# Kernel optimization log

Hardware: AMD Instinct MI355X
Metric: run time of the kernel (lower is better)

Reference implementation:

```python
import jax, jax.numpy as jnp
import numpy as np

B, S, E = 4, 2048, 1024


def setup_inputs() -> dict:
    key = jax.random.key(0)
    k1, k2, k3, k4 = jax.random.split(key, 4)
    scale = 1.0 / np.sqrt(E)
    return {
        "x": jax.random.normal(k1, (B, S, E), dtype=jnp.float32),
        "W_Q": jax.random.normal(k2, (E, E), dtype=jnp.float32) * scale,
        "W_K": jax.random.normal(k3, (E, E), dtype=jnp.float32) * scale,
        "W_V": jax.random.normal(k4, (E, E), dtype=jnp.float32) * scale,
    }


def reference(x, W_Q, W_K, W_V):
    # nn.Linear(E, E, bias=False): y = x @ W.T
    Q = jnp.einsum("bse,fe->bsf", x, W_Q)
    K = jnp.einsum("bse,fe->bsf", x, W_K)
    V = jnp.einsum("bse,fe->bsf", x, W_V)
    d = Q.shape[-1]
    scores = jnp.einsum("bqd,bkd->bqk", Q, K) / jnp.sqrt(jnp.float32(d))
    # causal mask: -inf strictly above the diagonal
    seq = Q.shape[1]
    causal = jnp.tril(jnp.ones((seq, seq), dtype=bool))  # [S,S]
    scores = jnp.where(causal[None, :, :], scores, jnp.float32(-jnp.inf))
    attn = jax.nn.softmax(scores, axis=-1)
    return jnp.einsum("bqk,bkd->bqd", attn, V)
```

## Files before the change

kernel.cpp:

```cpp
#include <hip/hip_runtime.h>
#include <hip/hip_bf16.h>
#include <stdint.h>

typedef __hip_bfloat16 bf16;
typedef __attribute__((ext_vector_type(8))) short bf16x8;
typedef __attribute__((ext_vector_type(4))) float f32x4;
typedef __attribute__((ext_vector_type(8))) unsigned short u16x8;
typedef __attribute__((ext_vector_type(4))) unsigned short u16x4;

#define SLEN 2048
#define ED   1024
#define NB   4
#define AS1 __attribute__((address_space(1)))
#define AS3 __attribute__((address_space(3)))
#define SB0() __builtin_amdgcn_sched_barrier(0)

static __device__ __forceinline__ unsigned short f2bf(float f) {
    return __builtin_bit_cast(unsigned short, __float2bfloat16(f));
}

__device__ __forceinline__ void gemm_core(
    const char* __restrict__ aT, int lda,
    const char* __restrict__ bT, int ldb,
    int nkt, char* sm, int tid, f32x4 (&acc)[4][4])
{
    const int lane = tid & 63, wave = tid >> 6;
    const int wm = wave >> 1, wn = wave & 1;
    const int fr = lane & 15, kc = lane >> 4;

    auto STAGE = [&](int kh, int Tn) {
        char* buf = sm + (Tn & 1) * 49152;
#pragma unroll
        for (int j = 0; j < 2; ++j) {
            int rid = j * 512 + tid;
            int row = rid >> 2, c = rid & 3;
            const char* src = aT + (size_t)row * lda + Tn * 128 + kh * 64
                            + ((c ^ ((row >> 1) & 3)) * 16);
            __builtin_amdgcn_global_load_lds(
                (const AS1 uint32_t*)src,
                (AS3 uint32_t*)(buf + kh * 16384 + (j * 512 + wave * 64) * 16),
                16, 0, 0);
        }
        {
            int row = tid >> 2, c = tid & 3;
            const char* src = bT + (size_t)row * ldb + Tn * 128 + kh * 64
                            + ((c ^ ((row >> 1) & 3)) * 16);
            __builtin_amdgcn_global_load_lds(
                (const AS1 uint32_t*)src,
                (AS3 uint32_t*)(buf + 32768 + kh * 8192 + (wave * 64) * 16),
                16, 0, 0);
        }
    };
    auto RD = [&](int T, int kh, bf16x8 (&a)[4], bf16x8 (&b)[4]) {
        const char* buf = sm + (T & 1) * 49152;
#pragma unroll
        for (int i = 0; i < 4; ++i) {
            int row = wm * 64 + i * 16 + fr;
            a[i] = *(const bf16x8*)(buf + kh * 16384 + row * 64
                                    + ((kc ^ ((row >> 1) & 3)) * 16));
        }
#pragma unroll
        for (int i = 0; i < 4; ++i) {
            int row = wn * 64 + i * 16 + fr;
            b[i] = *(const bf16x8*)(buf + 32768 + kh * 8192 + row * 64
                                    + ((kc ^ ((row >> 1) & 3)) * 16));
        }
    };
    auto MM = [&](bf16x8 (&a)[4], bf16x8 (&b)[4]) {
        __builtin_amdgcn_s_setprio(1);
#pragma unroll
        for (int i = 0; i < 4; ++i)
#pragma unroll
            for (int n = 0; n < 4; ++n)
                acc[i][n] = __builtin_amdgcn_mfma_f32_16x16x32_bf16(
                    a[i], b[n], acc[i][n], 0, 0, 0);
        __builtin_amdgcn_s_setprio(0);
    };

    STAGE(0, 0); STAGE(1, 0);
    asm volatile("s_waitcnt vmcnt(3)" ::: "memory");
    SB0();
    __builtin_amdgcn_s_barrier();

    bf16x8 aE[4], bE[4], aO[4], bO[4];
    for (int T = 0; T < nkt; ++T) {
        const bool pre = (T + 1 < nkt);
        RD(T, 0, aE, bE);
        SB0();
        if (pre) STAGE(0, T + 1);
        SB0();
        if (T > 0) {
            asm volatile("s_waitcnt lgkmcnt(8)" ::: "memory");
            SB0();
            MM(aO, bO);
        }
        if (pre) asm volatile("s_waitcnt vmcnt(3)" ::: "memory");
        else     asm volatile("s_waitcnt vmcnt(0)" ::: "memory");
        SB0();
        __builtin_amdgcn_s_barrier();
        RD(T, 1, aO, bO);
        SB0();
        if (pre) STAGE(1, T + 1);
        SB0();
        asm volatile("s_waitcnt lgkmcnt(8)" ::: "memory");
        SB0();
        MM(aE, bE);
        if (pre) asm volatile("s_waitcnt vmcnt(3)" ::: "memory");
        else     asm volatile("s_waitcnt vmcnt(0)" ::: "memory");
        SB0();
        __builtin_amdgcn_s_barrier();
    }
    asm volatile("s_waitcnt lgkmcnt(0)" ::: "memory");
    SB0();
    MM(aO, bO);
}

__global__ __launch_bounds__(256) void convert_to_bf16(
    const float* __restrict__ x, const float* __restrict__ wq,
    const float* __restrict__ wk, const float* __restrict__ wv,
    bf16* __restrict__ xb, bf16* __restrict__ wqb,
    bf16* __restrict__ wkb, bf16* __restrict__ wvb)
{
    long g = (long)blockIdx.x * 256 + threadIdx.x;
    const float* src; bf16* dst; long o;
    if (g < 1048576) { src = x; dst = xb; o = g * 8; }
    else {
        long g2 = g - 1048576;
        int w = (int)(g2 >> 17);
        o = (g2 & 131071) * 8;
        src = (w == 0) ? wq : (w == 1) ? wk : wv;
        dst = (w == 0) ? wqb : (w == 1) ? wkb : wvb;
    }
    float4 v0 = *(const float4*)(src + o);
    float4 v1 = *(const float4*)(src + o + 4);
    u16x8 r;
    r[0] = f2bf(v0.x); r[1] = f2bf(v0.y); r[2] = f2bf(v0.z); r[3] = f2bf(v0.w);
    r[4] = f2bf(v1.x); r[5] = f2bf(v1.y); r[6] = f2bf(v1.z); r[7] = f2bf(v1.w);
    *(u16x8*)(dst + o) = r;
}

__global__ __launch_bounds__(512, 2) void qkv_gemm(
    const bf16* __restrict__ xb, const bf16* __restrict__ wqb,
    const bf16* __restrict__ wkb, const bf16* __restrict__ wvb,
    bf16* __restrict__ Qb, bf16* __restrict__ Kb, bf16* __restrict__ Vt)
{
    extern __shared__ char smem[];
    int bid = blockIdx.x, tid = threadIdx.x;
    int xcd = bid & 7, i = bid >> 3;
    int tm = (xcd << 2) | (i & 3);
    int tn = i >> 2;
    const bf16* W = (tn < 8) ? wqb : (tn < 16) ? wkb : wvb;
    int tnl = tn & 7;
    f32x4 acc[4][4] = {};
    gemm_core((const char*)(xb + (size_t)tm * 256 * ED), ED * 2,
              (const char*)(W + (size_t)tnl * 128 * ED), ED * 2,
              16, smem, tid, acc);

    int lane = tid & 63, wave = tid >> 6, wm = wave >> 1, wn = wave & 1;
    int rl = (lane >> 4) * 4, cl = lane & 15;
    if (tn < 16) {
        bf16* C = (tn < 8) ? Qb : Kb;
#pragma unroll
        for (int mf = 0; mf < 4; ++mf)
#pragma unroll
            for (int j = 0; j < 4; ++j) {
                int r = tm * 256 + wm * 64 + mf * 16 + rl + j;
#pragma unroll
                for (int nf = 0; nf < 4; ++nf) {
                    int c = tnl * 128 + wn * 64 + nf * 16 + cl;
                    C[(size_t)r * ED + c] = __float2bfloat16(acc[mf][nf][j]);
                }
            }
    } else {
#pragma unroll
        for (int mf = 0; mf < 4; ++mf)
#pragma unroll
            for (int j = 0; j < 4; ++j) {
                int r = tm * 256 + wm * 64 + mf * 16 + rl + j;
                int bb = r >> 11, s = r & 2047;
#pragma unroll
                for (int nf = 0; nf < 4; ++nf) {
                    int d = tnl * 128 + wn * 64 + nf * 16 + cl;
                    Vt[(((size_t)bb << 10) + d) * SLEN + s] = __float2bfloat16(acc[mf][nf][j]);
                }
            }
    }
}

__global__ __launch_bounds__(512, 2) void qk_gemm(
    const bf16* __restrict__ Qb, const bf16* __restrict__ Kb, float* __restrict__ Sc)
{
    extern __shared__ char smem[];
    int bx = blockIdx.x, b = blockIdx.y, tid = threadIdx.x;
    int t = (bx & 7) * 9 + (bx >> 3);
    int ti = 0;
    while ((ti + 1) * (ti + 2) <= t) ++ti;
    int tj = t - ti * (ti + 1);
    f32x4 acc[4][4] = {};
    gemm_core((const char*)(Qb + ((size_t)b * SLEN + ti * 256) * ED), ED * 2,
              (const char*)(Kb + ((size_t)b * SLEN + tj * 128) * ED), ED * 2,
              16, smem, tid, acc);

    float* Sb = Sc + (size_t)b * SLEN * SLEN;
    int lane = tid & 63, wave = tid >> 6, wm = wave >> 1, wn = wave & 1;
    int rl = (lane >> 4) * 4, cl = lane & 15;
#pragma unroll
    for (int mf = 0; mf < 4; ++mf)
#pragma unroll
        for (int j = 0; j < 4; ++j) {
            int r = ti * 256 + wm * 64 + mf * 16 + rl + j;
#pragma unroll
            for (int nf = 0; nf < 4; ++nf) {
                int c = tj * 128 + wn * 64 + nf * 16 + cl;
                Sb[(size_t)r * SLEN + c] = acc[mf][nf][j] * 0.03125f;
            }
        }
}

__global__ __launch_bounds__(256) void softmax_rows(float* __restrict__ Sc)
{
    int q = blockIdx.x, b = blockIdx.y, tid = threadIdx.x;
    float* row = Sc + ((size_t)b * SLEN + q) * SLEN;
    int lane = tid & 63, wave = tid >> 6;
    __shared__ float red[4];

    float vals[8];
    float lmax = -3.0e38f;
#pragma unroll
    for (int r = 0; r < 2; ++r) {
        int i4 = tid + r * 256;
        if (i4 * 4 <= q) {
            float4 v = *(const float4*)(row + i4 * 4);
            vals[r * 4 + 0] = v.x; vals[r * 4 + 1] = v.y;
            vals[r * 4 + 2] = v.z; vals[r * 4 + 3] = v.w;
#pragma unroll
            for (int e = 0; e < 4; ++e) {
                int k = i4 * 4 + e;
                if (k <= q) lmax = fmaxf(lmax, vals[r * 4 + e]);
            }
        }
    }
#pragma unroll
    for (int o = 32; o > 0; o >>= 1) lmax = fmaxf(lmax, __shfl_xor(lmax, o));
    if (lane == 0) red[wave] = lmax;
    __syncthreads();
    float m = fmaxf(fmaxf(red[0], red[1]), fmaxf(red[2], red[3]));
    __syncthreads();
    float lsum = 0.f;
#pragma unroll
    for (int r = 0; r < 2; ++r) {
        int i4 = tid + r * 256;
        if (i4 * 4 <= q)
#pragma unroll
            for (int e = 0; e < 4; ++e) {
                int k = i4 * 4 + e;
                if (k <= q) lsum += __expf(vals[r * 4 + e] - m);
            }
    }
#pragma unroll
    for (int o = 32; o > 0; o >>= 1) lsum += __shfl_xor(lsum, o);
    if (lane == 0) red[wave] = lsum;
    __syncthreads();
    float inv = 1.0f / (red[0] + red[1] + red[2] + red[3]);
    unsigned short* prow = (unsigned short*)row;
#pragma unroll
    for (int r = 0; r < 2; ++r) {
        int i4 = tid + r * 256;
        u16x4 o4;
#pragma unroll
        for (int e = 0; e < 4; ++e) {
            int k = i4 * 4 + e;
            float p = (k <= q) ? __expf(vals[r * 4 + e] - m) * inv : 0.0f;
            o4[e] = f2bf(p);
        }
        *(u16x4*)(prow + i4 * 4) = o4;
    }
}

__global__ __launch_bounds__(512, 2) void pv_gemm(
    const bf16* __restrict__ P, const bf16* __restrict__ Vt, float* __restrict__ O)
{
    extern __shared__ char smem[];
    int mq = 7 - blockIdx.x, nd = blockIdx.y, b = blockIdx.z, tid = threadIdx.x;
    f32x4 acc[4][4] = {};
    int nkt = (mq + 1) * 4;
    gemm_core((const char*)P + ((size_t)b * SLEN + mq * 256) * 8192, 8192,
              (const char*)(Vt + ((size_t)b * ED + nd * 128) * SLEN), SLEN * 2,
              nkt, smem, tid, acc);

    int lane = tid & 63, wave = tid >> 6, wm = wave >> 1, wn = wave & 1;
    int rl = (lane >> 4) * 4, cl = lane & 15;
    float* Ob = O + (size_t)b * SLEN * ED;
#pragma unroll
    for (int mf = 0; mf < 4; ++mf)
#pragma unroll
        for (int j = 0; j < 4; ++j) {
            int r = mq * 256 + wm * 64 + mf * 16 + rl + j;
#pragma unroll
            for (int nf = 0; nf < 4; ++nf) {
                int c = nd * 128 + wn * 64 + nf * 16 + cl;
                Ob[(size_t)r * ED + c] = acc[mf][nf][j];
            }
        }
}

extern "C" void kernel_launch(void* const* d_in, const int* in_sizes, int n_in,
                              void* d_out, int out_size, void* d_ws, size_t ws_size,
                              hipStream_t stream)
{
    const float* x  = (const float*)d_in[0];
    const float* wq = (const float*)d_in[1];
    const float* wk = (const float*)d_in[2];
    const float* wv = (const float*)d_in[3];
    float* out = (float*)d_out;

    char* ws = (char*)d_ws;
    bf16* xb  = (bf16*)(ws);
    bf16* wqb = (bf16*)(ws + 16777216);
    bf16* wkb = (bf16*)(ws + 18874368);
    bf16* wvb = (bf16*)(ws + 20971520);
    bf16* Qb  = (bf16*)(ws + 23068672);
    bf16* Kb  = (bf16*)(ws + 39845888);
    bf16* Vt  = (bf16*)(ws + 56623104);
    float* Sc = (float*)(ws + 73400320);

    (void)hipFuncSetAttribute((const void*)qkv_gemm,
            hipFuncAttributeMaxDynamicSharedMemorySize, 98304);
    (void)hipFuncSetAttribute((const void*)qk_gemm,
            hipFuncAttributeMaxDynamicSharedMemorySize, 98304);
    (void)hipFuncSetAttribute((const void*)pv_gemm,
            hipFuncAttributeMaxDynamicSharedMemorySize, 98304);

    convert_to_bf16<<<5632, 256, 0, stream>>>(x, wq, wk, wv, xb, wqb, wkb, wvb);
    qkv_gemm<<<768, 512, 98304, stream>>>(xb, wqb, wkb, wvb, Qb, Kb, Vt);
    qk_gemm<<<dim3(72, NB), 512, 98304, stream>>>(Qb, Kb, Sc);
    softmax_rows<<<dim3(SLEN, NB), 256, 0, stream>>>(Sc);
    pv_gemm<<<dim3(8, 8, NB), 512, 98304, stream>>>((const bf16*)Sc, Vt, out);
}
```

Before: 155.1 us.

## Rebalance causal PV GEMM with smaller tiles and an atomic work queue

Replaces the 256x128, 512-thread PV GEMM with a 128x128, 256-thread variant that has its own two-stage LDS pipeline (gemm2p). Blocks pull tiles from a global atomic counter, heaviest causal rows first, to cut the load imbalance from triangular work. The counter lives in the no-longer-needed W_K bf16 workspace slot and is reset by an extra memset each call. Smaller tiles lower per-tile data reuse and add atomic and barrier overhead.

```diff
diff --git a/kernel.cpp b/kernel.cpp
--- a/kernel.cpp
+++ b/kernel.cpp
@@ -19,7 +19,7 @@
     return __builtin_bit_cast(unsigned short, __float2bfloat16(f));
 }
 
-__device__ __forceinline__ void gemm_core(
+__device__ __forceinline__ void gemm_core8(
     const char* __restrict__ aT, int lda,
     const char* __restrict__ bT, int ldb,
     int nkt, char* sm, int tid, f32x4 (&acc)[4][4])
@@ -115,6 +115,79 @@
     MM(aO, bO);
 }
 
+__device__ __forceinline__ void gemm2p(
+    const char* __restrict__ aT, int lda,
+    const char* __restrict__ bT, int ldb,
+    int nkt, char* sm, int tid, f32x4 (&acc)[4][4])
+{
+    const int lane = tid & 63, wave = tid >> 6;
+    const int wm = wave >> 1, wn = wave & 1;
+    const int fr = lane & 15, kc = lane >> 4;
+
+    auto STAGE = [&](int kh, int Tn) {
+        char* base = sm + (Tn & 1) * 32768 + kh * 8192;
+#pragma unroll
+        for (int half = 0; half < 2; ++half) {
+            const char* g = half ? bT : aT;
+            const int ld = half ? ldb : lda;
+            char* pb = base + half * 16384;
+#pragma unroll
+            for (int j = 0; j < 2; ++j) {
+                int rid = j * 256 + tid;
+                int row = rid >> 2, c = rid & 3;
+                const char* src = g + (size_t)row * ld + Tn * 128 + kh * 64
+                                + ((c ^ ((row >> 1) & 3)) * 16);
+                __builtin_amdgcn_global_load_lds(
+                    (const AS1 uint32_t*)src,
+                    (AS3 uint32_t*)(pb + (j * 256 + wave * 64) * 16),
+                    16, 0, 0);
+            }
+        }
+    };
+
+    STAGE(0, 0); STAGE(1, 0);
+    asm volatile("s_waitcnt vmcnt(4)" ::: "memory");
+    __builtin_amdgcn_sched_barrier(0);
+    __builtin_amdgcn_s_barrier();
+
+    for (int T = 0; T < nkt; ++T) {
+        const bool pre = (T + 1 < nkt);
+#pragma unroll
+        for (int kh = 0; kh < 2; ++kh) {
+            const char* buf = sm + (T & 1) * 32768 + kh * 8192;
+            bf16x8 a[4], b[4];
+#pragma unroll
+            for (int i = 0; i < 4; ++i) {
+                int row = wm * 64 + i * 16 + fr;
+                a[i] = *(const bf16x8*)(buf + row * 64 + ((kc ^ ((row >> 1) & 3)) * 16));
+            }
+#pragma unroll
+            for (int i = 0; i < 4; ++i) {
+                int row = wn * 64 + i * 16 + fr;
+                b[i] = *(const bf16x8*)(buf + 16384 + row * 64 + ((kc ^ ((row >> 1) & 3)) * 16));
+            }
+            if (pre) {
+                STAGE(kh, T + 1);
+                asm volatile("s_waitcnt vmcnt(4)" ::: "memory");
+            } else {
+                asm volatile("s_waitcnt vmcnt(0)" ::: "memory");
+            }
+            __builtin_amdgcn_sched_barrier(0);
+            __builtin_amdgcn_s_barrier();
+            asm volatile("s_waitcnt lgkmcnt(0)" ::: "memory");
+            __builtin_amdgcn_sched_barrier(0);
+            __builtin_amdgcn_s_setprio(1);
+#pragma unroll
+            for (int i = 0; i < 4; ++i)
+#pragma unroll
+                for (int n = 0; n < 4; ++n)
+                    acc[i][n] = __builtin_amdgcn_mfma_f32_16x16x32_bf16(
+                        a[i], b[n], acc[i][n], 0, 0, 0);
+            __builtin_amdgcn_s_setprio(0);
+        }
+    }
+}
+
 __global__ __launch_bounds__(256) void convert_to_bf16(
     const float* __restrict__ x, const float* __restrict__ wq,
     const float* __restrict__ wk, const float* __restrict__ wv,
@@ -152,9 +225,9 @@
     const bf16* W = (tn < 8) ? wqb : (tn < 16) ? wkb : wvb;
     int tnl = tn & 7;
     f32x4 acc[4][4] = {};
-    gemm_core((const char*)(xb + (size_t)tm * 256 * ED), ED * 2,
-              (const char*)(W + (size_t)tnl * 128 * ED), ED * 2,
-              16, smem, tid, acc);
+    gemm_core8((const char*)(xb + (size_t)tm * 256 * ED), ED * 2,
+               (const char*)(W + (size_t)tnl * 128 * ED), ED * 2,
+               16, smem, tid, acc);
 
     int lane = tid & 63, wave = tid >> 6, wm = wave >> 1, wn = wave & 1;
     int rl = (lane >> 4) * 4, cl = lane & 15;
@@ -197,9 +270,9 @@
     while ((ti + 1) * (ti + 2) <= t) ++ti;
     int tj = t - ti * (ti + 1);
     f32x4 acc[4][4] = {};
-    gemm_core((const char*)(Qb + ((size_t)b * SLEN + ti * 256) * ED), ED * 2,
-              (const char*)(Kb + ((size_t)b * SLEN + tj * 128) * ED), ED * 2,
-              16, smem, tid, acc);
+    gemm_core8((const char*)(Qb + ((size_t)b * SLEN + ti * 256) * ED), ED * 2,
+               (const char*)(Kb + ((size_t)b * SLEN + tj * 128) * ED), ED * 2,
+               16, smem, tid, acc);
 
     float* Sb = Sc + (size_t)b * SLEN * SLEN;
     int lane = tid & 63, wave = tid >> 6, wm = wave >> 1, wn = wave & 1;
@@ -277,31 +350,42 @@
     }
 }
 
-__global__ __launch_bounds__(512, 2) void pv_gemm(
-    const bf16* __restrict__ P, const bf16* __restrict__ Vt, float* __restrict__ O)
+__global__ __launch_bounds__(256, 2) void pv_gemm(
+    const bf16* __restrict__ P, const bf16* __restrict__ Vt,
+    float* __restrict__ O, int* __restrict__ ctr)
 {
     extern __shared__ char smem[];
-    int mq = 7 - blockIdx.x, nd = blockIdx.y, b = blockIdx.z, tid = threadIdx.x;
-    f32x4 acc[4][4] = {};
-    int nkt = (mq + 1) * 4;
-    gemm_core((const char*)P + ((size_t)b * SLEN + mq * 256) * 8192, 8192,
-              (const char*)(Vt + ((size_t)b * ED + nd * 128) * SLEN), SLEN * 2,
-              nkt, smem, tid, acc);
-
-    int lane = tid & 63, wave = tid >> 6, wm = wave >> 1, wn = wave & 1;
-    int rl = (lane >> 4) * 4, cl = lane & 15;
-    float* Ob = O + (size_t)b * SLEN * ED;
-#pragma unroll
-    for (int mf = 0; mf < 4; ++mf)
-#pragma unroll
-        for (int j = 0; j < 4; ++j) {
-            int r = mq * 256 + wm * 64 + mf * 16 + rl + j;
-#pragma unroll
-            for (int nf = 0; nf < 4; ++nf) {
-                int c = nd * 128 + wn * 64 + nf * 16 + cl;
-                Ob[(size_t)r * ED + c] = acc[mf][nf][j];
-            }
-        }
+    __shared__ int tsh;
+    int tid = threadIdx.x;
+    for (;;) {
+        __syncthreads();
+        if (tid == 0) tsh = atomicAdd(ctr, 1);
+        __syncthreads();
+        int t = tsh;
+        if (t >= 512) break;
+        int mq = 15 - (t >> 5), sub = t & 31;
+        int nd = sub >> 2, b = sub & 3;
+        f32x4 acc[4][4] = {};
+        int nkt = (mq + 1) * 2;
+        gemm2p((const char*)P + ((size_t)b * SLEN + mq * 128) * 8192, 8192,
+               (const char*)(Vt + ((size_t)b * ED + nd * 128) * SLEN), SLEN * 2,
+               nkt, smem, tid, acc);
+
+        int lane = tid & 63, wave = tid >> 6, wm = wave >> 1, wn = wave & 1;
+        int rl = (lane >> 4) * 4, cl = lane & 15;
+        float* Ob = O + (size_t)b * SLEN * ED;
+#pragma unroll
+        for (int mf = 0; mf < 4; ++mf)
+#pragma unroll
+            for (int j = 0; j < 4; ++j) {
+                int r = mq * 128 + wm * 64 + mf * 16 + rl + j;
+#pragma unroll
+                for (int nf = 0; nf < 4; ++nf) {
+                    int c = nd * 128 + wn * 64 + nf * 16 + cl;
+                    Ob[(size_t)r * ED + c] = acc[mf][nf][j];
+                }
+            }
+    }
 }
 
 extern "C" void kernel_launch(void* const* d_in, const int* in_sizes, int n_in,
@@ -323,17 +407,19 @@
     bf16* Kb  = (bf16*)(ws + 39845888);
     bf16* Vt  = (bf16*)(ws + 56623104);
     float* Sc = (float*)(ws + 73400320);
+    int*  ctr = (int*)(ws + 18874368);
 
     (void)hipFuncSetAttribute((const void*)qkv_gemm,
             hipFuncAttributeMaxDynamicSharedMemorySize, 98304);
     (void)hipFuncSetAttribute((const void*)qk_gemm,
             hipFuncAttributeMaxDynamicSharedMemorySize, 98304);
     (void)hipFuncSetAttribute((const void*)pv_gemm,
-            hipFuncAttributeMaxDynamicSharedMemorySize, 98304);
+            hipFuncAttributeMaxDynamicSharedMemorySize, 65536);
 
     convert_to_bf16<<<5632, 256, 0, stream>>>(x, wq, wk, wv, xb, wqb, wkb, wvb);
     qkv_gemm<<<768, 512, 98304, stream>>>(xb, wqb, wkb, wvb, Qb, Kb, Vt);
     qk_gemm<<<dim3(72, NB), 512, 98304, stream>>>(Qb, Kb, Sc);
     softmax_rows<<<dim3(SLEN, NB), 256, 0, stream>>>(Sc);
-    pv_gemm<<<dim3(8, 8, NB), 512, 98304, stream>>>((const bf16*)Sc, Vt, out);
-}
+    (void)hipMemsetAsync(ctr, 0, sizeof(int), stream);
+    pv_gemm<<<512, 256, 65536, stream>>>((const bf16*)Sc, Vt, out, ctr);
+}
```

New measurement: 235.9 us. 52.1% more time.

## Use 256x256 tiles with 8-phase pipelined GEMM for QKV and QK kernels

Applied to the files above, without the earlier changes.

Adds a new GEMM core that computes 256x256 output tiles per block, with 8 waves each owning 128x64, and interleaves LDS reads, MFMA and async global-to-LDS staging across sub-phases with barriers and priority hints. The QKV projection and QK score kernels switch to this core, halving their grid sizes and using 128KB of shared memory. The aim is higher arithmetic intensity per LDS byte and better overlap of loads with compute. In exchange, occupancy drops to one block per CU, and the QK causal tiling now computes full 256-wide diagonal tiles.

```diff
diff --git a/kernel.cpp b/kernel.cpp
--- a/kernel.cpp
+++ b/kernel.cpp
@@ -19,7 +19,100 @@
     return __builtin_bit_cast(unsigned short, __float2bfloat16(f));
 }
 
-__device__ __forceinline__ void gemm_core(
+__device__ __forceinline__ void gemm8p(
+    const char* __restrict__ aT, int lda,
+    const char* __restrict__ bT, int ldb,
+    int nkt, char* sm, int tid, f32x4 (&acc)[8][4])
+{
+    const int lane = tid & 63, wave = tid >> 6;
+    const int wm = wave >> 2, wn = wave & 3;
+    const int fr = lane & 15, kc = lane >> 4;
+
+    auto SU = [&](int isB, int kh, int Tn) {
+        char* dst = sm + (Tn & 1) * 65536 + isB * 32768 + kh * 16384;
+        const char* g = isB ? bT : aT;
+        const int ld = isB ? ldb : lda;
+#pragma unroll
+        for (int j = 0; j < 2; ++j) {
+            int rid = j * 512 + tid;
+            int row = rid >> 2, c = rid & 3;
+            const char* src = g + (size_t)row * ld + Tn * 128 + kh * 64
+                            + ((c ^ ((row >> 1) & 3)) * 16);
+            __builtin_amdgcn_global_load_lds(
+                (const AS1 uint32_t*)src,
+                (AS3 uint32_t*)(dst + (j * 512 + wave * 64) * 16), 16, 0, 0);
+        }
+    };
+    auto RDA = [&](int T, int kh, bf16x8 (&a)[8]) {
+        const char* pa = sm + (T & 1) * 65536 + kh * 16384;
+#pragma unroll
+        for (int i = 0; i < 8; ++i) {
+            int row = wm * 128 + i * 16 + fr;
+            a[i] = *(const bf16x8*)(pa + row * 64 + ((kc ^ ((row >> 1) & 3)) * 16));
+        }
+    };
+    auto RDB = [&](int T, int kh, int nh, bf16x8 (&b)[2]) {
+        const char* pb = sm + (T & 1) * 65536 + 32768 + kh * 16384;
+#pragma unroll
+        for (int n = 0; n < 2; ++n) {
+            int row = wn * 64 + nh * 32 + n * 16 + fr;
+            b[n] = *(const bf16x8*)(pb + row * 64 + ((kc ^ ((row >> 1) & 3)) * 16));
+        }
+    };
+    auto MM = [&](bf16x8 (&a)[8], bf16x8 (&b)[2], int nh) {
+        __builtin_amdgcn_s_setprio(1);
+#pragma unroll
+        for (int i = 0; i < 8; ++i)
+#pragma unroll
+            for (int n = 0; n < 2; ++n)
+                acc[i][nh * 2 + n] = __builtin_amdgcn_mfma_f32_16x16x32_bf16(
+                    a[i], b[n], acc[i][nh * 2 + n], 0, 0, 0);
+        __builtin_amdgcn_s_setprio(0);
+    };
+
+    SU(0, 0, 0); SU(1, 0, 0); SU(0, 1, 0); SU(1, 1, 0);
+    SU(0, 0, 1); SU(1, 0, 1); SU(0, 1, 1);
+    asm volatile("s_waitcnt vmcnt(6)" ::: "memory");
+    SB0();
+    __builtin_amdgcn_s_barrier();
+
+    for (int T = 0; T < nkt; ++T) {
+        const bool p1 = (T + 1 < nkt), p2 = (T + 2 < nkt);
+        bf16x8 a[8], b[2];
+        RDA(T, 0, a); RDB(T, 0, 0, b);
+        if (p1) SU(1, 1, T + 1);
+        SB0(); __builtin_amdgcn_s_barrier();
+        asm volatile("s_waitcnt lgkmcnt(0)" ::: "memory");
+        SB0();
+        MM(a, b, 0);
+        SB0(); __builtin_amdgcn_s_barrier();
+        RDB(T, 0, 1, b);
+        if (p2) SU(0, 0, T + 2);
+        SB0(); __builtin_amdgcn_s_barrier();
+        asm volatile("s_waitcnt lgkmcnt(0)" ::: "memory");
+        SB0();
+        MM(a, b, 1);
+        SB0(); __builtin_amdgcn_s_barrier();
+        RDA(T, 1, a); RDB(T, 1, 0, b);
+        if (p2) SU(1, 0, T + 2);
+        SB0(); __builtin_amdgcn_s_barrier();
+        asm volatile("s_waitcnt lgkmcnt(0)" ::: "memory");
+        SB0();
+        MM(a, b, 0);
+        SB0(); __builtin_amdgcn_s_barrier();
+        RDB(T, 1, 1, b);
+        if (p2) SU(0, 1, T + 2);
+        if (T < nkt - 2) asm volatile("s_waitcnt vmcnt(6)" ::: "memory");
+        else             asm volatile("s_waitcnt vmcnt(0)" ::: "memory");
+        SB0(); __builtin_amdgcn_s_barrier();
+        asm volatile("s_waitcnt lgkmcnt(0)" ::: "memory");
+        SB0();
+        MM(a, b, 1);
+        SB0(); __builtin_amdgcn_s_barrier();
+    }
+}
+
+__device__ __forceinline__ void gemm_core8(
     const char* __restrict__ aT, int lda,
     const char* __restrict__ bT, int ldb,
     int nkt, char* sm, int tid, f32x4 (&acc)[4][4])
@@ -149,38 +242,38 @@
     int xcd = bid & 7, i = bid >> 3;
     int tm = (xcd << 2) | (i & 3);
     int tn = i >> 2;
-    const bf16* W = (tn < 8) ? wqb : (tn < 16) ? wkb : wvb;
-    int tnl = tn & 7;
-    f32x4 acc[4][4] = {};
-    gemm_core((const char*)(xb + (size_t)tm * 256 * ED), ED * 2,
-              (const char*)(W + (size_t)tnl * 128 * ED), ED * 2,
-              16, smem, tid, acc);
-
-    int lane = tid & 63, wave = tid >> 6, wm = wave >> 1, wn = wave & 1;
+    const bf16* W = (tn < 4) ? wqb : (tn < 8) ? wkb : wvb;
+    int tnl = tn & 3;
+    f32x4 acc[8][4] = {};
+    gemm8p((const char*)(xb + (size_t)tm * 256 * ED), ED * 2,
+           (const char*)(W + (size_t)tnl * 256 * ED), ED * 2,
+           16, smem, tid, acc);
+
+    int lane = tid & 63, wave = tid >> 6, wm = wave >> 2, wn = wave & 3;
     int rl = (lane >> 4) * 4, cl = lane & 15;
-    if (tn < 16) {
-        bf16* C = (tn < 8) ? Qb : Kb;
-#pragma unroll
-        for (int mf = 0; mf < 4; ++mf)
+    if (tn < 8) {
+        bf16* C = (tn < 4) ? Qb : Kb;
+#pragma unroll
+        for (int mf = 0; mf < 8; ++mf)
 #pragma unroll
             for (int j = 0; j < 4; ++j) {
-                int r = tm * 256 + wm * 64 + mf * 16 + rl + j;
+                int r = tm * 256 + wm * 128 + mf * 16 + rl + j;
 #pragma unroll
                 for (int nf = 0; nf < 4; ++nf) {
-                    int c = tnl * 128 + wn * 64 + nf * 16 + cl;
+                    int c = tnl * 256 + wn * 64 + nf * 16 + cl;
                     C[(size_t)r * ED + c] = __float2bfloat16(acc[mf][nf][j]);
                 }
             }
     } else {
 #pragma unroll
-        for (int mf = 0; mf < 4; ++mf)
+        for (int mf = 0; mf < 8; ++mf)
 #pragma unroll
             for (int j = 0; j < 4; ++j) {
-                int r = tm * 256 + wm * 64 + mf * 16 + rl + j;
+                int r = tm * 256 + wm * 128 + mf * 16 + rl + j;
                 int bb = r >> 11, s = r & 2047;
 #pragma unroll
                 for (int nf = 0; nf < 4; ++nf) {
-                    int d = tnl * 128 + wn * 64 + nf * 16 + cl;
+                    int d = tnl * 256 + wn * 64 + nf * 16 + cl;
                     Vt[(((size_t)bb << 10) + d) * SLEN + s] = __float2bfloat16(acc[mf][nf][j]);
                 }
             }
@@ -191,27 +284,26 @@
     const bf16* __restrict__ Qb, const bf16* __restrict__ Kb, float* __restrict__ Sc)
 {
     extern __shared__ char smem[];
-    int bx = blockIdx.x, b = blockIdx.y, tid = threadIdx.x;
-    int t = (bx & 7) * 9 + (bx >> 3);
+    int t = blockIdx.x, b = blockIdx.y, tid = threadIdx.x;
     int ti = 0;
-    while ((ti + 1) * (ti + 2) <= t) ++ti;
-    int tj = t - ti * (ti + 1);
-    f32x4 acc[4][4] = {};
-    gemm_core((const char*)(Qb + ((size_t)b * SLEN + ti * 256) * ED), ED * 2,
-              (const char*)(Kb + ((size_t)b * SLEN + tj * 128) * ED), ED * 2,
-              16, smem, tid, acc);
+    while ((ti + 1) * (ti + 2) / 2 <= t) ++ti;
+    int tj = t - ti * (ti + 1) / 2;
+    f32x4 acc[8][4] = {};
+    gemm8p((const char*)(Qb + ((size_t)b * SLEN + ti * 256) * ED), ED * 2,
+           (const char*)(Kb + ((size_t)b * SLEN + tj * 256) * ED), ED * 2,
+           16, smem, tid, acc);
 
     float* Sb = Sc + (size_t)b * SLEN * SLEN;
-    int lane = tid & 63, wave = tid >> 6, wm = wave >> 1, wn = wave & 1;
+    int lane = tid & 63, wave = tid >> 6, wm = wave >> 2, wn = wave & 3;
     int rl = (lane >> 4) * 4, cl = lane & 15;
 #pragma unroll
-    for (int mf = 0; mf < 4; ++mf)
+    for (int mf = 0; mf < 8; ++mf)
 #pragma unroll
         for (int j = 0; j < 4; ++j) {
-            int r = ti * 256 + wm * 64 + mf * 16 + rl + j;
+            int r = ti * 256 + wm * 128 + mf * 16 + rl + j;
 #pragma unroll
             for (int nf = 0; nf < 4; ++nf) {
-                int c = tj * 128 + wn * 64 + nf * 16 + cl;
+                int c = tj * 256 + wn * 64 + nf * 16 + cl;
                 Sb[(size_t)r * SLEN + c] = acc[mf][nf][j] * 0.03125f;
             }
         }
@@ -284,9 +376,9 @@
     int mq = 7 - blockIdx.x, nd = blockIdx.y, b = blockIdx.z, tid = threadIdx.x;
     f32x4 acc[4][4] = {};
     int nkt = (mq + 1) * 4;
-    gemm_core((const char*)P + ((size_t)b * SLEN + mq * 256) * 8192, 8192,
-              (const char*)(Vt + ((size_t)b * ED + nd * 128) * SLEN), SLEN * 2,
-              nkt, smem, tid, acc);
+    gemm_core8((const char*)P + ((size_t)b * SLEN + mq * 256) * 8192, 8192,
+               (const char*)(Vt + ((size_t)b * ED + nd * 128) * SLEN), SLEN * 2,
+               nkt, smem, tid, acc);
 
     int lane = tid & 63, wave = tid >> 6, wm = wave >> 1, wn = wave & 1;
     int rl = (lane >> 4) * 4, cl = lane & 15;
@@ -325,15 +417,15 @@
     float* Sc = (float*)(ws + 73400320);
 
     (void)hipFuncSetAttribute((const void*)qkv_gemm,
-            hipFuncAttributeMaxDynamicSharedMemorySize, 98304);
+            hipFuncAttributeMaxDynamicSharedMemorySize, 131072);
     (void)hipFuncSetAttribute((const void*)qk_gemm,
-            hipFuncAttributeMaxDynamicSharedMemorySize, 98304);
+            hipFuncAttributeMaxDynamicSharedMemorySize, 131072);
     (void)hipFuncSetAttribute((const void*)pv_gemm,
             hipFuncAttributeMaxDynamicSharedMemorySize, 98304);
 
     convert_to_bf16<<<5632, 256, 0, stream>>>(x, wq, wk, wv, xb, wqb, wkb, wvb);
-    qkv_gemm<<<768, 512, 98304, stream>>>(xb, wqb, wkb, wvb, Qb, Kb, Vt);
-    qk_gemm<<<dim3(72, NB), 512, 98304, stream>>>(Qb, Kb, Sc);
+    qkv_gemm<<<384, 512, 131072, stream>>>(xb, wqb, wkb, wvb, Qb, Kb, Vt);
+    qk_gemm<<<dim3(36, NB), 512, 131072, stream>>>(Qb, Kb, Sc);
     softmax_rows<<<dim3(SLEN, NB), 256, 0, stream>>>(Sc);
     pv_gemm<<<dim3(8, 8, NB), 512, 98304, stream>>>((const bf16*)Sc, Vt, out);
 }
```

New measurement: 163.8 us. +5.6%, slower.
